# Optimization experiments

Measured on AMD Instinct MI355X. Metric: run time of the kernel, lower is better.

The kernel has to match this reference:

```python
import jax, jax.numpy as jnp
import numpy as np

L, N, C = 1024, 32, 512
EPS = 1e-5

def _linear(y, W, b):
    # torch nn.Linear: y @ W.T + b ; y: (L,N,C), W: (C,C)
    return jnp.einsum('lnc,dc->lnd', y, W) + b

def _bn(y, gamma, beta):
    # training-mode BatchNorm1d over (N, C, L) -> stats per channel over (L, N)
    m = y.mean(axis=(0, 1))
    v = y.var(axis=(0, 1))  # biased variance, as torch uses for normalization
    return (y - m) * jax.lax.rsqrt(v + EPS) * gamma + beta

def _indrnn(y, u):
    # h_t = relu(x_t + u * h_{t-1}), elementwise per-channel recurrence over L
    h0 = jnp.zeros(y.shape[1:], y.dtype)
    def step(h, xt):
        h = jax.nn.relu(xt + u * h)
        return h, h
    _, hs = jax.lax.scan(step, h0, y)
    return hs

def setup_inputs() -> dict:
    key = jax.random.key(0)
    ks = jax.random.split(key, 12)
    s = 1.0 / np.sqrt(C)
    x = jax.random.normal(ks[0], (L, N, C), dtype=jnp.float32)
    W1 = jax.random.uniform(ks[1], (C, C), jnp.float32, -s, s)
    b1 = jax.random.uniform(ks[2], (C,), jnp.float32, -s, s)
    g1 = jnp.ones((C,), jnp.float32)
    be1 = jnp.zeros((C,), jnp.float32)
    u1 = jax.random.uniform(ks[3], (C,), jnp.float32, 0.0, 1.0)
    W2 = jax.random.uniform(ks[4], (C, C), jnp.float32, -s, s)
    b2 = jax.random.uniform(ks[5], (C,), jnp.float32, -s, s)
    g2 = jnp.ones((C,), jnp.float32)
    be2 = jnp.zeros((C,), jnp.float32)
    u2 = jax.random.uniform(ks[6], (C,), jnp.float32, 0.0, 1.0)
    return {"x": x, "W1": W1, "b1": b1, "g1": g1, "be1": be1, "u1": u1,
            "W2": W2, "b2": b2, "g2": g2, "be2": be2, "u2": u2}

def reference(x, W1, b1, g1, be1, u1, W2, b2, g2, be2, u2):
    # linear_first=True branch; dropout=0.0 -> identity
    y = _linear(x, W1, b1)
    y = _bn(y, g1, be1)
    y = _indrnn(y, u1)
    y = _linear(y, W2, b2)
    y = _bn(y, g2, be2)
    y = _indrnn(y, u2)
    return y + x
```

## Files before the change

### kernel.cpp

```cpp
#include <hip/hip_runtime.h>
#include <stdint.h>

#define L_DIM 1024
#define N_DIM 32
#define C_DIM 512
#define M_DIM (L_DIM * N_DIM)
#define EPS_BN 1e-5f

typedef __attribute__((ext_vector_type(8))) short bf16x8;
typedef __attribute__((ext_vector_type(4))) float f32x4;

__device__ __forceinline__ unsigned short f2bf(float f) {
  union { float f; unsigned int u; } a; a.f = f;
  unsigned int u = a.u;
  return (unsigned short)((u + 0x7FFFu + ((u >> 16) & 1u)) >> 16);
}
__device__ __forceinline__ float bf2f(unsigned short h) {
  union { float f; unsigned int u; } a; a.u = ((unsigned int)h) << 16;
  return a.f;
}

__device__ __forceinline__ void gl16(const void* g, void* l) {
  __builtin_amdgcn_global_load_lds(
      (const __attribute__((address_space(1))) unsigned int*)g,
      (__attribute__((address_space(3))) unsigned int*)l, 16, 0, 0);
}

__global__ void k_split_all(const float* __restrict__ x, const float* __restrict__ W1,
                            const float* __restrict__ W2,
                            unsigned short* __restrict__ Ahi,
                            unsigned short* __restrict__ W1hi,
                            unsigned short* __restrict__ W2hi) {
  const int NX = M_DIM * C_DIM / 4;
  const int NW = C_DIM * C_DIM / 4;
  int i = blockIdx.x * 256 + threadIdx.x;
  int stride = gridDim.x * 256;
  for (; i < NX + 2 * NW; i += stride) {
    const float4* src; unsigned short* dh; int j;
    if (i < NX)            { src = (const float4*)x;  dh = Ahi;  j = i; }
    else if (i < NX + NW)  { src = (const float4*)W1; dh = W1hi; j = i - NX; }
    else                   { src = (const float4*)W2; dh = W2hi; j = i - NX - NW; }
    float4 v = src[j];
    ushort4 h;
    h.x = f2bf(v.x); h.y = f2bf(v.y); h.z = f2bf(v.z); h.w = f2bf(v.w);
    ((ushort4*)dh)[j] = h;
  }
}

__global__ __launch_bounds__(256, 4)
void k_gemm(const unsigned short* __restrict__ A,
            const unsigned short* __restrict__ B,
            const float* __restrict__ bias, unsigned short* __restrict__ C,
            float* __restrict__ gsum, float* __restrict__ gsq) {
  const int K = C_DIM;
  int d = blockIdx.x;
  int xcd = d & 7;
  int q = d >> 3;
  int bm = xcd * 32 + (q >> 2);
  int bn = q & 3;

  __shared__ unsigned short lds[2][8192];

  int tid  = threadIdx.x;
  int lane = tid & 63;
  int wave = tid >> 6;
  int wm = wave >> 1;
  int wn = wave & 1;
  int lr = lane & 15;
  int lk = lane >> 4;

  f32x4 acc[4][4];
#pragma unroll
  for (int i = 0; i < 4; ++i)
#pragma unroll
    for (int j = 0; j < 4; ++j) acc[i][j] = (f32x4){0.f, 0.f, 0.f, 0.f};

  const int ra = tid & 127, ka = tid >> 7;
  const int oa0 = (bm * 128 + ra) * K + ka * 8;
  const int oa1 = (bm * 128 + ra) * K + (ka + 2) * 8;
  const int ob0 = (bn * 128 + ra) * K + ka * 8;
  const int ob1 = (bn * 128 + ra) * K + (ka + 2) * 8;

#define STAGE(buf, kk)                                          \
  do {                                                          \
    unsigned short* Lb = lds[buf];                              \
    gl16(A + oa0 + (kk), Lb + (tid) * 8);                       \
    gl16(A + oa1 + (kk), Lb + (tid + 256) * 8);                 \
    gl16(B + ob0 + (kk), Lb + (tid + 512) * 8);                 \
    gl16(B + ob1 + (kk), Lb + (tid + 768) * 8);                 \
  } while (0)

#define COMPUTE(buf)                                                          \
  do {                                                                        \
    const unsigned short* Lb = lds[buf];                                      \
    bf16x8 bh[4], af[4];                                                      \
    _Pragma("unroll")                                                         \
    for (int nj = 0; nj < 4; ++nj) {                                          \
      int slot = 512 + lk * 128 + wn * 64 + nj * 16 + lr;                     \
      bh[nj] = *(const bf16x8*)(Lb + slot * 8);                               \
    }                                                                         \
    _Pragma("unroll")                                                         \
    for (int mi = 0; mi < 4; ++mi) {                                          \
      int slot = lk * 128 + wm * 64 + mi * 16 + lr;                           \
      af[mi] = *(const bf16x8*)(Lb + slot * 8);                               \
    }                                                                         \
    _Pragma("unroll")                                                         \
    for (int mi = 0; mi < 4; ++mi)                                            \
      _Pragma("unroll")                                                       \
      for (int nj = 0; nj < 4; ++nj)                                          \
        acc[mi][nj] = __builtin_amdgcn_mfma_f32_16x16x32_bf16(af[mi], bh[nj], acc[mi][nj], 0, 0, 0); \
  } while (0)

  const int nt = K >> 5;
  STAGE(0, 0);
  STAGE(1, 32);

  for (int t = 0; t < nt - 1; ++t) {
    asm volatile("s_waitcnt vmcnt(4)" ::: "memory");
    __builtin_amdgcn_sched_barrier(0);
    __builtin_amdgcn_s_barrier();
    COMPUTE(t & 1);
    __builtin_amdgcn_s_barrier();
    if (t < nt - 2) STAGE(t & 1, (t + 2) << 5);
  }
  asm volatile("s_waitcnt vmcnt(0)" ::: "memory");
  __builtin_amdgcn_sched_barrier(0);
  __builtin_amdgcn_s_barrier();
  COMPUTE((nt - 1) & 1);

#pragma unroll
  for (int nj = 0; nj < 4; ++nj) {
    int gn = bn * 128 + wn * 64 + nj * 16 + lr;
    float bv = bias[gn];
    float s = 0.f, qq = 0.f;
#pragma unroll
    for (int mi = 0; mi < 4; ++mi) {
      int gm = bm * 128 + wm * 64 + mi * 16 + (lk << 2);
#pragma unroll
      for (int r = 0; r < 4; ++r) {
        float v = acc[mi][nj][r] + bv;
        C[(gm + r) * C_DIM + gn] = f2bf(v);
        s += v; qq += v * v;
      }
    }
    s  += __shfl_xor(s, 16);  qq += __shfl_xor(qq, 16);
    s  += __shfl_xor(s, 32);  qq += __shfl_xor(qq, 32);
    if (lk == 0) {
      atomicAdd(&gsum[gn], s);
      atomicAdd(&gsq[gn], qq);
    }
  }
#undef STAGE
#undef COMPUTE
}


__global__ __launch_bounds__(1024, 4)
void k_indrnn_split(const unsigned short* __restrict__ y,
                    const float* __restrict__ gsum, const float* __restrict__ gsq,
                    const float* __restrict__ g, const float* __restrict__ be,
                    const float* __restrict__ u,
                    unsigned short* __restrict__ hhi) {
  __shared__ float tA[1024], tB[1024], tM[1024];
  int lane = threadIdx.x & 63;
  int w = threadIdx.x >> 6;
  int chain = blockIdx.x * 64 + lane;
  int c = chain & 511;
  float m  = gsum[c] * (1.0f / (float)M_DIM);
  float vv = gsq[c]  * (1.0f / (float)M_DIM) - m * m;
  float sc = g[c] * rsqrtf(vv + EPS_BN);
  float sh = be[c] - m * sc;
  float uu = u[c];
  const unsigned short* py = y + chain;
  const int base = w * 64;

  float A = 0.f, Bc = 1.f, Mx = 0.f;
  for (int c0 = 0; c0 < 64; c0 += 16) {
    float vb[16];
#pragma unroll
    for (int i = 0; i < 16; ++i) vb[i] = bf2f(py[(base + c0 + i) * 16384]);
#pragma unroll
    for (int i = 0; i < 16; ++i) {
      float xt = fmaf(vb[i], sc, sh);
      A  = fmaf(uu, A, xt);
      Mx = fmaxf(fmaf(uu, Mx, xt), 0.f);
      Bc *= uu;
    }
  }
  tA[w * 64 + lane] = A; tB[w * 64 + lane] = Bc; tM[w * 64 + lane] = Mx;
  __syncthreads();

  float pA = 0.f, pM = 0.f;
  for (int s = 0; s < w; ++s) {
    float a = tA[s * 64 + lane], b = tB[s * 64 + lane], mm = tM[s * 64 + lane];
    pA = fmaf(b, pA, a);
    pM = fmaxf(fmaf(b, pM, a), mm);
  }
  float h = fmaxf(pA, pM);

  unsigned short* ph = hhi + chain;
  for (int c0 = 0; c0 < 64; c0 += 16) {
    float vb[16];
#pragma unroll
    for (int i = 0; i < 16; ++i) vb[i] = bf2f(py[(base + c0 + i) * 16384]);
#pragma unroll
    for (int i = 0; i < 16; ++i) {
      float xt = fmaf(vb[i], sc, sh);
      h = fmaxf(fmaf(uu, h, xt), 0.f);
      ph[(base + c0 + i) * 16384] = f2bf(h);
    }
  }
}

__global__ __launch_bounds__(1024, 4)
void k_indrnn_res(const unsigned short* __restrict__ y, const float* __restrict__ x,
                  float* __restrict__ outp,
                  const float* __restrict__ gsum, const float* __restrict__ gsq,
                  const float* __restrict__ g, const float* __restrict__ be,
                  const float* __restrict__ u) {
  __shared__ float tA[1024], tB[1024], tM[1024];
  int lane = threadIdx.x & 63;
  int w = threadIdx.x >> 6;
  int chain = blockIdx.x * 64 + lane;
  int c = chain & 511;
  float m  = gsum[c] * (1.0f / (float)M_DIM);
  float vv = gsq[c]  * (1.0f / (float)M_DIM) - m * m;
  float sc = g[c] * rsqrtf(vv + EPS_BN);
  float sh = be[c] - m * sc;
  float uu = u[c];
  const unsigned short* py = y + chain;
  const float* px = x + chain;
  float* po = outp + chain;
  const int base = w * 64;

  float A = 0.f, Bc = 1.f, Mx = 0.f;
  for (int c0 = 0; c0 < 64; c0 += 16) {
    float vb[16];
#pragma unroll
    for (int i = 0; i < 16; ++i) vb[i] = bf2f(py[(base + c0 + i) * 16384]);
#pragma unroll
    for (int i = 0; i < 16; ++i) {
      float xt = fmaf(vb[i], sc, sh);
      A  = fmaf(uu, A, xt);
      Mx = fmaxf(fmaf(uu, Mx, xt), 0.f);
      Bc *= uu;
    }
  }
  tA[w * 64 + lane] = A; tB[w * 64 + lane] = Bc; tM[w * 64 + lane] = Mx;
  __syncthreads();

  float pA = 0.f, pM = 0.f;
  for (int s = 0; s < w; ++s) {
    float a = tA[s * 64 + lane], b = tB[s * 64 + lane], mm = tM[s * 64 + lane];
    pA = fmaf(b, pA, a);
    pM = fmaxf(fmaf(b, pM, a), mm);
  }
  float h = fmaxf(pA, pM);

  for (int c0 = 0; c0 < 64; c0 += 16) {
    float vb[16], xb[16];
#pragma unroll
    for (int i = 0; i < 16; ++i) vb[i] = bf2f(py[(base + c0 + i) * 16384]);
#pragma unroll
    for (int i = 0; i < 16; ++i) xb[i] = px[(base + c0 + i) * 16384];
#pragma unroll
    for (int i = 0; i < 16; ++i) {
      float xt = fmaf(vb[i], sc, sh);
      h = fmaxf(fmaf(uu, h, xt), 0.f);
      po[(base + c0 + i) * 16384] = h + xb[i];
    }
  }
}

extern "C" void kernel_launch(void* const* d_in, const int* in_sizes, int n_in,
                              void* d_out, int out_size, void* d_ws, size_t ws_size,
                              hipStream_t stream) {
  if (n_in < 11) return;
  const float* x   = (const float*)d_in[0];
  const float* W1  = (const float*)d_in[1];
  const float* b1  = (const float*)d_in[2];
  const float* g1  = (const float*)d_in[3];
  const float* be1 = (const float*)d_in[4];
  const float* u1  = (const float*)d_in[5];
  const float* W2  = (const float*)d_in[6];
  const float* b2  = (const float*)d_in[7];
  const float* g2  = (const float*)d_in[8];
  const float* be2 = (const float*)d_in[9];
  const float* u2  = (const float*)d_in[10];
  float* out = (float*)d_out;

  char* ws = (char*)d_ws;
  const size_t SZ_HALF = (size_t)M_DIM * C_DIM * sizeof(unsigned short);
  const size_t SZ_W    = (size_t)C_DIM * C_DIM * sizeof(unsigned short);
  unsigned short* Ahi  = (unsigned short*)(ws);
  unsigned short* Cbf  = (unsigned short*)(ws + SZ_HALF);
  unsigned short* W1hi = (unsigned short*)(ws + 2 * SZ_HALF);
  unsigned short* W2hi = W1hi + C_DIM * C_DIM;
  float* stats = (float*)(ws + 2 * SZ_HALF + 2 * SZ_W);
  float* sum1 = stats,        *sq1 = stats + 512;
  float* sum2 = stats + 1024, *sq2 = stats + 1536;
  if (ws_size < 2 * SZ_HALF + 2 * SZ_W + 4 * 512 * sizeof(float)) return;

  hipMemsetAsync(stats, 0, 4 * 512 * sizeof(float), stream);

  k_split_all<<<2048, 256, 0, stream>>>(x, W1, W2, Ahi, W1hi, W2hi);

  dim3 gemmGrid(1024);
  k_gemm<<<gemmGrid, 256, 0, stream>>>(Ahi, W1hi, b1, Cbf, sum1, sq1);
  k_indrnn_split<<<256, 1024, 0, stream>>>(Cbf, sum1, sq1, g1, be1, u1, Ahi);

  k_gemm<<<gemmGrid, 256, 0, stream>>>(Ahi, W2hi, b2, Cbf, sum2, sq2);
  k_indrnn_res<<<256, 1024, 0, stream>>>(Cbf, x, out, sum2, sq2, g2, be2, u2);
}
```

Measured before the change: 158.5 us.

## Triple-buffer GEMM K-loop and stage epilogue through LDS for coalesced bf16 stores

The GEMM main loop moves from double to triple buffering in LDS, with a fully unrolled round schedule that waits on vmcnt(8), so two tiles of global-to-LDS loads stay in flight while each tile is computed. The epilogue now writes bias-added results into LDS in two halves, then reads them back as 16-byte rows to emit coalesced bf16x8 global stores instead of scattered 2-byte stores. The cost is more LDS per block (48KB), a lower occupancy hint in the launch bounds, and extra barriers in the epilogue.

Result: no change. 158.4 us (-0.0%).

```diff
diff --git a/kernel.cpp b/kernel.cpp
--- a/kernel.cpp
+++ b/kernel.cpp
@@ -47,7 +47,7 @@
   }
 }
 
-__global__ __launch_bounds__(256, 4)
+__global__ __launch_bounds__(256, 2)
 void k_gemm(const unsigned short* __restrict__ A,
             const unsigned short* __restrict__ B,
             const float* __restrict__ bias, unsigned short* __restrict__ C,
@@ -59,7 +59,7 @@
   int bm = xcd * 32 + (q >> 2);
   int bn = q & 3;
 
-  __shared__ unsigned short lds[2][8192];
+  __shared__ unsigned short lds[3][8192];
 
   int tid  = threadIdx.x;
   int lane = tid & 63;
@@ -75,11 +75,12 @@
 #pragma unroll
     for (int j = 0; j < 4; ++j) acc[i][j] = (f32x4){0.f, 0.f, 0.f, 0.f};
 
-  const int ra = tid & 127, ka = tid >> 7;
-  const int oa0 = (bm * 128 + ra) * K + ka * 8;
-  const int oa1 = (bm * 128 + ra) * K + (ka + 2) * 8;
-  const int ob0 = (bn * 128 + ra) * K + ka * 8;
-  const int ob1 = (bn * 128 + ra) * K + (ka + 2) * 8;
+  const int r0 = tid & 127;
+  const int kc0 = tid >> 7;
+  const int oa0 = (bm * 128 + r0) * K + (kc0 + 0) * 8;
+  const int oa1 = (bm * 128 + r0) * K + (kc0 + 2) * 8;
+  const int ob0 = (bn * 128 + r0) * K + (kc0 + 0) * 8;
+  const int ob1 = (bn * 128 + r0) * K + (kc0 + 2) * 8;
 
 #define STAGE(buf, kk)                                          \
   do {                                                          \
@@ -111,47 +112,93 @@
         acc[mi][nj] = __builtin_amdgcn_mfma_f32_16x16x32_bf16(af[mi], bh[nj], acc[mi][nj], 0, 0, 0); \
   } while (0)
 
-  const int nt = K >> 5;
+#define ROUND(b, kknext)                                        \
+  do {                                                          \
+    asm volatile("s_waitcnt vmcnt(8)" ::: "memory");            \
+    __builtin_amdgcn_sched_barrier(0);                          \
+    __builtin_amdgcn_s_barrier();                               \
+    COMPUTE(b);                                                 \
+    __builtin_amdgcn_s_barrier();                               \
+    STAGE(b, (kknext));                                         \
+  } while (0)
+
   STAGE(0, 0);
   STAGE(1, 32);
-
-  for (int t = 0; t < nt - 1; ++t) {
-    asm volatile("s_waitcnt vmcnt(4)" ::: "memory");
-    __builtin_amdgcn_sched_barrier(0);
-    __builtin_amdgcn_s_barrier();
-    COMPUTE(t & 1);
-    __builtin_amdgcn_s_barrier();
-    if (t < nt - 2) STAGE(t & 1, (t + 2) << 5);
-  }
+  STAGE(2, 64);
+
+#pragma unroll
+  for (int tb = 0; tb < 12; tb += 3) {
+    ROUND(0, (tb + 3) << 5);
+    ROUND(1, (tb + 4) << 5);
+    ROUND(2, (tb + 5) << 5);
+  }
+  ROUND(0, 15 << 5);
+  asm volatile("s_waitcnt vmcnt(8)" ::: "memory");
+  __builtin_amdgcn_sched_barrier(0);
+  __builtin_amdgcn_s_barrier();
+  COMPUTE(1);
+  __builtin_amdgcn_s_barrier();
+  asm volatile("s_waitcnt vmcnt(4)" ::: "memory");
+  __builtin_amdgcn_sched_barrier(0);
+  __builtin_amdgcn_s_barrier();
+  COMPUTE(2);
+  __builtin_amdgcn_s_barrier();
   asm volatile("s_waitcnt vmcnt(0)" ::: "memory");
   __builtin_amdgcn_sched_barrier(0);
   __builtin_amdgcn_s_barrier();
-  COMPUTE((nt - 1) & 1);
-
-#pragma unroll
-  for (int nj = 0; nj < 4; ++nj) {
-    int gn = bn * 128 + wn * 64 + nj * 16 + lr;
-    float bv = bias[gn];
-    float s = 0.f, qq = 0.f;
-#pragma unroll
-    for (int mi = 0; mi < 4; ++mi) {
-      int gm = bm * 128 + wm * 64 + mi * 16 + (lk << 2);
-#pragma unroll
-      for (int r = 0; r < 4; ++r) {
-        float v = acc[mi][nj][r] + bv;
-        C[(gm + r) * C_DIM + gn] = f2bf(v);
-        s += v; qq += v * v;
+  COMPUTE(0);
+
+  __syncthreads();
+  float* T = (float*)&lds[0][0];
+#pragma unroll
+  for (int half = 0; half < 2; ++half) {
+    if (wm == half) {
+#pragma unroll
+      for (int nj = 0; nj < 4; ++nj) {
+        int gn = bn * 128 + wn * 64 + nj * 16 + lr;
+        float bv = bias[gn];
+        float s = 0.f, qq = 0.f;
+        int lcol = wn * 64 + nj * 16 + lr;
+#pragma unroll
+        for (int mi = 0; mi < 4; ++mi) {
+          int lrow = mi * 16 + (lk << 2);
+#pragma unroll
+          for (int r = 0; r < 4; ++r) {
+            float v = acc[mi][nj][r] + bv;
+            T[(lrow + r) * 128 + lcol] = v;
+            s += v; qq += v * v;
+          }
+        }
+        s  += __shfl_xor(s, 16);  qq += __shfl_xor(qq, 16);
+        s  += __shfl_xor(s, 32);  qq += __shfl_xor(qq, 32);
+        if (lk == 0) {
+          atomicAdd(&gsum[gn], s);
+          atomicAdd(&gsq[gn], qq);
+        }
       }
     }
-    s  += __shfl_xor(s, 16);  qq += __shfl_xor(qq, 16);
-    s  += __shfl_xor(s, 32);  qq += __shfl_xor(qq, 32);
-    if (lk == 0) {
-      atomicAdd(&gsum[gn], s);
-      atomicAdd(&gsq[gn], qq);
-    }
+    __syncthreads();
+    {
+      int rr = tid >> 4, jj = tid & 15;
+#pragma unroll
+      for (int i = 0; i < 4; ++i) {
+        int row = i * 16 + rr;
+        const float* src = T + row * 128 + jj * 8;
+        f32x4 a0 = *(const f32x4*)src;
+        f32x4 a1 = *(const f32x4*)(src + 4);
+        union { unsigned int u[4]; bf16x8 v; } P;
+        P.u[0] = (unsigned int)f2bf(a0[0]) | ((unsigned int)f2bf(a0[1]) << 16);
+        P.u[1] = (unsigned int)f2bf(a0[2]) | ((unsigned int)f2bf(a0[3]) << 16);
+        P.u[2] = (unsigned int)f2bf(a1[0]) | ((unsigned int)f2bf(a1[1]) << 16);
+        P.u[3] = (unsigned int)f2bf(a1[2]) | ((unsigned int)f2bf(a1[3]) << 16);
+        *(bf16x8*)(C + (size_t)(bm * 128 + half * 64 + row) * C_DIM + bn * 128 + jj * 8) = P.v;
+      }
+    }
+    __syncthreads();
   }
 #undef STAGE
 #undef COMPUTE
+#undef ROUND
 }
 
 
```
